# Kernel optimization log

Measured on AMD Instinct MI355X. Metric: run time of the kernel, lower is better.

Reference implementation:

```python
import jax, jax.numpy as jnp
import numpy as np

M_MARGIN = 0.5
S_SCALE = 30.0
EPS = 1e-12

def _l2norm(a):
    return a / jnp.maximum(jnp.linalg.norm(a, axis=1, keepdims=True), EPS)

def setup_inputs() -> dict:
    key = jax.random.key(0)
    k1, k2, k3 = jax.random.split(key, 3)
    B, D, V = 2048, 512, 32000
    x = jax.random.normal(k1, (B, D), dtype=jnp.float32)
    # kaiming_normal_ on (V, D): std = sqrt(2 / D)
    W = jax.random.normal(k2, (V, D), dtype=jnp.float32) * np.sqrt(2.0 / D)
    labels = jax.random.randint(k3, (B,), 0, V, dtype=jnp.int64)
    return {"x": x, "W": W, "labels": labels}

def reference(x, W, labels):
    cos_m, sin_m = jnp.cos(M_MARGIN), jnp.sin(M_MARGIN)
    nx = _l2norm(x)            # [B, D]
    nW = _l2norm(W)            # [V, D]
    cosine = nx @ nW.T         # [B, V]
    B = cosine.shape[0]
    rows = jnp.arange(B)
    # phi only matters at the label column (phi.where(one_hot, cosine))
    cos_y = cosine[rows, labels]                            # [B]
    sin_y = jnp.sqrt(jnp.clip(1.0 - cos_y * cos_y, 0.0, 1.0))
    phi_y = cos_y * cos_m - sin_y * sin_m                   # [B]
    logits = cosine.at[rows, labels].set(phi_y) * S_SCALE   # [B, V]
    logp = jax.nn.log_softmax(logits, axis=1)
    return -logp[rows, labels].sum() / B
```

## Files before the change

### kernel.cpp

```cpp
#include <hip/hip_runtime.h>
#include <math.h>
#include <stdint.h>

#define B_ROWS 2048
#define D_DIM  512
#define V_COLS 32000
#define BM 128
#define BN 128
#define BK 64
#define KSTEPS (D_DIM / BK)
#define NCT    (V_COLS / BN)
#define S_SC   30.0f
#define COS_M  0.8775825618903728f
#define SIN_M  0.479425538604203f

typedef float f32x4 __attribute__((ext_vector_type(4)));
typedef long  i64x2 __attribute__((ext_vector_type(2)));

__device__ __forceinline__ void load16_to_lds(const void* g, void* l) {
  __builtin_amdgcn_global_load_lds(
      (__attribute__((address_space(1))) void*)(g),
      (__attribute__((address_space(3))) void*)(l),
      16, 0, 0);
}

__global__ void fused_norm_kernel(const float* __restrict__ x,
                                  const float* __restrict__ W,
                                  uint8_t* __restrict__ nx,
                                  uint8_t* __restrict__ nw,
                                  float* __restrict__ rowsum,
                                  float* __restrict__ out) {
  if (blockIdx.x == 0 && threadIdx.x == 0) out[0] = 0.f;
  if (blockIdx.x < B_ROWS / 256) rowsum[blockIdx.x * 256 + threadIdx.x] = 0.f;
  const int lane = threadIdx.x & 63;
  const int wave = threadIdx.x >> 6;
  const int gr   = blockIdx.x * 4 + wave;
  const float* src;
  uint8_t* dst;
  if (gr < B_ROWS) {
    src = x + (size_t)gr * D_DIM;
    dst = nx + (size_t)gr * D_DIM;
  } else {
    src = W + (size_t)(gr - B_ROWS) * D_DIM;
    dst = nw + (size_t)(gr - B_ROWS) * D_DIM;
  }
  const float4* r4 = (const float4*)src;
  float4 v0 = r4[2 * lane];
  float4 v1 = r4[2 * lane + 1];
  float ss = v0.x*v0.x + v0.y*v0.y + v0.z*v0.z + v0.w*v0.w
           + v1.x*v1.x + v1.y*v1.y + v1.z*v1.z + v1.w*v1.w;
  #pragma unroll
  for (int off = 32; off >= 1; off >>= 1) ss += __shfl_xor(ss, off, 64);
  float inv = 1.0f / fmaxf(sqrtf(ss), 1e-12f);
  int p0 = __builtin_amdgcn_cvt_pk_fp8_f32(v0.x * inv, v0.y * inv, 0, false);
  p0     = __builtin_amdgcn_cvt_pk_fp8_f32(v0.z * inv, v0.w * inv, p0, true);
  int p1 = __builtin_amdgcn_cvt_pk_fp8_f32(v1.x * inv, v1.y * inv, 0, false);
  p1     = __builtin_amdgcn_cvt_pk_fp8_f32(v1.z * inv, v1.w * inv, p1, true);
  ((int2*)dst)[lane] = make_int2(p0, p1);
}

__global__ __launch_bounds__(256, 4)
void arc_gemm_kernel(const uint8_t* __restrict__ nx,
                     const uint8_t* __restrict__ nw,
                     const int* __restrict__ labels,
                     float* __restrict__ rowsum,
                     float* __restrict__ lbl_logit) {
  __shared__ uint8_t sA[2][BM * BK];
  __shared__ uint8_t sB[2][BN * BK];

  const int id = blockIdx.x;
  const int ct = ((id >> 7) << 3) | (id & 7);
  if (ct >= NCT) return;
  const int rt = (id >> 3) & 15;
  const int m0 = rt * BM;
  const int n0 = ct * BN;

  const int tid  = threadIdx.x;
  const int wave = tid >> 6;
  const int lane = tid & 63;
  const int wm   = wave >> 1;
  const int wn   = wave & 1;
  const int quad = lane >> 4;
  const int l16  = lane & 15;

  const int srow = tid >> 2;
  const int jg   = (tid & 3) ^ ((srow >> 1) & 3);
  const uint8_t* gA = nx + (size_t)(m0 + srow) * D_DIM + jg * 16;
  const uint8_t* gB = nw + (size_t)(n0 + srow) * D_DIM + jg * 16;
  const int ldsOff0 = wave * 1024;
  const int ldsOff1 = 4096 + wave * 1024;

  const int cSlot = (quad ^ ((l16 >> 1) & 3)) << 4;
  const int aBase = (wm * 64 + l16) * BK + cSlot;
  const int bBase = (wn * 64 + l16) * BK + cSlot;

  f32x4 acc[4][4];
  #pragma unroll
  for (int i = 0; i < 4; ++i)
    #pragma unroll
    for (int j = 0; j < 4; ++j) acc[i][j] = (f32x4){0.f, 0.f, 0.f, 0.f};

  load16_to_lds(gA,              &sA[0][ldsOff0]);
  load16_to_lds(gA + 64 * D_DIM, &sA[0][ldsOff1]);
  load16_to_lds(gB,              &sB[0][ldsOff0]);
  load16_to_lds(gB + 64 * D_DIM, &sB[0][ldsOff1]);

  #pragma unroll
  for (int ks = 0; ks < KSTEPS; ++ks) {
    __syncthreads();
    if (ks + 1 < KSTEPS) {
      const int off = (ks + 1) * BK;
      const int nb  = (ks + 1) & 1;
      load16_to_lds(gA + off,              &sA[nb][ldsOff0]);
      load16_to_lds(gA + 64 * D_DIM + off, &sA[nb][ldsOff1]);
      load16_to_lds(gB + off,              &sB[nb][ldsOff0]);
      load16_to_lds(gB + 64 * D_DIM + off, &sB[nb][ldsOff1]);
    }
    __syncthreads();

    const uint8_t* bA = sA[ks & 1];
    const uint8_t* bB = sB[ks & 1];
    i64x2 a2[4];
    #pragma unroll
    for (int mi = 0; mi < 4; ++mi)
      a2[mi] = *(const i64x2*)(bA + aBase + mi * 16 * BK);
    #pragma unroll
    for (int ni = 0; ni < 4; ++ni) {
      const i64x2 b2 = *(const i64x2*)(bB + bBase + ni * 16 * BK);
      #pragma unroll
      for (int mi = 0; mi < 4; ++mi) {
        acc[mi][ni] = __builtin_amdgcn_mfma_f32_16x16x32_fp8_fp8(a2[mi][0], b2[0], acc[mi][ni], 0, 0, 0);
        acc[mi][ni] = __builtin_amdgcn_mfma_f32_16x16x32_fp8_fp8(a2[mi][1], b2[1], acc[mi][ni], 0, 0, 0);
      }
    }
  }

  const int lblv = labels[m0 + wm * 64 + lane];
  #pragma unroll
  for (int mi = 0; mi < 4; ++mi) {
    #pragma unroll
    for (int r = 0; r < 4; ++r) {
      const int rw   = mi * 16 + quad * 4 + r;
      const int grow = m0 + wm * 64 + rw;
      const int lbl  = __shfl(lblv, rw, 64);
      float rsum = 0.f;
      #pragma unroll
      for (int ni = 0; ni < 4; ++ni) {
        float c = acc[mi][ni][r];
        const int gcol = n0 + wn * 64 + ni * 16 + l16;
        if (gcol == lbl) {
          float sy  = sqrtf(fminf(1.f, fmaxf(0.f, 1.f - c * c)));
          float phi = c * COS_M - sy * SIN_M;
          lbl_logit[grow] = S_SC * phi;
          c = phi;
        }
        rsum += __expf(S_SC * c - 30.0f);
      }
      #pragma unroll
      for (int off = 1; off < 16; off <<= 1)
        rsum += __shfl_xor(rsum, off, 64);
      if (l16 == 0) atomicAdd(&rowsum[grow], rsum);
    }
  }
}

__global__ void arc_finish_kernel(const float* __restrict__ rowsum,
                                  const float* __restrict__ lbl_logit,
                                  float* __restrict__ out) {
  const int row  = blockIdx.x * 256 + threadIdx.x;
  const int lane = threadIdx.x & 63;
  const int wave = threadIdx.x >> 6;
  float v = (30.0f + logf(rowsum[row]) - lbl_logit[row]) * (1.0f / (float)B_ROWS);
  #pragma unroll
  for (int off = 32; off >= 1; off >>= 1) v += __shfl_xor(v, off, 64);
  __shared__ float wsum[4];
  if (lane == 0) wsum[wave] = v;
  __syncthreads();
  if (threadIdx.x == 0) atomicAdd(out, wsum[0] + wsum[1] + wsum[2] + wsum[3]);
}

extern "C" void kernel_launch(void* const* d_in, const int* in_sizes, int n_in,
                              void* d_out, int out_size, void* d_ws, size_t ws_size,
                              hipStream_t stream) {
  const float* x      = (const float*)d_in[0];
  const float* W      = (const float*)d_in[1];
  const int*   labels = (const int*)d_in[2];
  float* out = (float*)d_out;

  char* ws = (char*)d_ws;
  uint8_t* nx = (uint8_t*)ws;
  uint8_t* nw = (uint8_t*)(ws + (size_t)B_ROWS * D_DIM);
  char* p = ws + (size_t)B_ROWS * D_DIM + (size_t)V_COLS * D_DIM;
  float* rowsum    = (float*)p;  p += (size_t)B_ROWS * 4;
  float* lbl_logit = (float*)p;

  hipLaunchKernelGGL(fused_norm_kernel, dim3((B_ROWS + V_COLS) / 4), dim3(256), 0, stream,
                     x, W, nx, nw, rowsum, out);
  hipLaunchKernelGGL(arc_gemm_kernel, dim3(32 * 16 * 8), dim3(256), 0, stream,
                     nx, nw, labels, rowsum, lbl_logit);
  hipLaunchKernelGGL(arc_finish_kernel, dim3(B_ROWS / 256), dim3(256), 0, stream,
                     rowsum, lbl_logit, out);
}
```

Baseline: 175.2 us.

## Switch GEMM to 32x32x64 scaled FP8 MFMA with 32-wide fragments

Replaces the 16x16x32 fp8 MFMA inner loop (32 instructions per k-step per wave) with four 32x32x64 mfma_scale f8f6f4 instructions, loading 32-byte A/B fragments from the swizzled LDS. The epilogue is remapped to the 32x32 accumulator layout, with a wider shuffle reduction and fewer atomics per row. Launch bounds drop to 3 blocks/SM to fit the larger register footprint. The aim is higher MFMA throughput and fewer LDS reads, at the cost of occupancy and a riskier fragment layout.

After: 295.2 us. 1.68x slower.

```diff
diff --git a/kernel.cpp b/kernel.cpp
--- a/kernel.cpp
+++ b/kernel.cpp
@@ -14,8 +14,9 @@
 #define COS_M  0.8775825618903728f
 #define SIN_M  0.479425538604203f
 
-typedef float f32x4 __attribute__((ext_vector_type(4)));
-typedef long  i64x2 __attribute__((ext_vector_type(2)));
+typedef float f32x16 __attribute__((ext_vector_type(16)));
+typedef int   i32x4v __attribute__((ext_vector_type(4)));
+typedef int   i32x8v __attribute__((ext_vector_type(8)));
 
 __device__ __forceinline__ void load16_to_lds(const void* g, void* l) {
   __builtin_amdgcn_global_load_lds(
@@ -59,7 +60,7 @@
   ((int2*)dst)[lane] = make_int2(p0, p1);
 }
 
-__global__ __launch_bounds__(256, 4)
+__global__ __launch_bounds__(256, 3)
 void arc_gemm_kernel(const uint8_t* __restrict__ nx,
                      const uint8_t* __restrict__ nw,
                      const int* __restrict__ labels,
@@ -80,8 +81,8 @@
   const int lane = tid & 63;
   const int wm   = wave >> 1;
   const int wn   = wave & 1;
-  const int quad = lane >> 4;
-  const int l16  = lane & 15;
+  const int c31  = lane & 31;
+  const int h    = lane >> 5;
 
   const int srow = tid >> 2;
   const int jg   = (tid & 3) ^ ((srow >> 1) & 3);
@@ -90,15 +91,18 @@
   const int ldsOff0 = wave * 1024;
   const int ldsOff1 = 4096 + wave * 1024;
 
-  const int cSlot = (quad ^ ((l16 >> 1) & 3)) << 4;
-  const int aBase = (wm * 64 + l16) * BK + cSlot;
-  const int bBase = (wn * 64 + l16) * BK + cSlot;
-
-  f32x4 acc[4][4];
-  #pragma unroll
-  for (int i = 0; i < 4; ++i)
+  const int swz  = (c31 >> 1) & 3;
+  const int s0   = ((2 * h) ^ swz) << 4;
+  const int aA0  = (wm * 64 + c31) * BK + s0;
+  const int bB0  = (wn * 64 + c31) * BK + s0;
+
+  f32x16 acc[2][2];
+  #pragma unroll
+  for (int i = 0; i < 2; ++i)
     #pragma unroll
-    for (int j = 0; j < 4; ++j) acc[i][j] = (f32x4){0.f, 0.f, 0.f, 0.f};
+    for (int j = 0; j < 2; ++j)
+      #pragma unroll
+      for (int g = 0; g < 16; ++g) acc[i][j][g] = 0.f;
 
   load16_to_lds(gA,              &sA[0][ldsOff0]);
   load16_to_lds(gA + 64 * D_DIM, &sA[0][ldsOff1]);
@@ -120,34 +124,39 @@
 
     const uint8_t* bA = sA[ks & 1];
     const uint8_t* bB = sB[ks & 1];
-    i64x2 a2[4];
+
+    i32x4v a0l = *(const i32x4v*)(bA + aA0);
+    i32x4v a0h = *(const i32x4v*)(bA + (aA0 ^ 16));
+    i32x4v a1l = *(const i32x4v*)(bA + aA0 + 32 * BK);
+    i32x4v a1h = *(const i32x4v*)(bA + ((aA0 + 32 * BK) ^ 16));
+    i32x4v b0l = *(const i32x4v*)(bB + bB0);
+    i32x4v b0h = *(const i32x4v*)(bB + (bB0 ^ 16));
+    i32x4v b1l = *(const i32x4v*)(bB + bB0 + 32 * BK);
+    i32x4v b1h = *(const i32x4v*)(bB + ((bB0 + 32 * BK) ^ 16));
+    i32x8v aF0 = __builtin_shufflevector(a0l, a0h, 0, 1, 2, 3, 4, 5, 6, 7);
+    i32x8v aF1 = __builtin_shufflevector(a1l, a1h, 0, 1, 2, 3, 4, 5, 6, 7);
+    i32x8v bF0 = __builtin_shufflevector(b0l, b0h, 0, 1, 2, 3, 4, 5, 6, 7);
+    i32x8v bF1 = __builtin_shufflevector(b1l, b1h, 0, 1, 2, 3, 4, 5, 6, 7);
+
+    acc[0][0] = __builtin_amdgcn_mfma_scale_f32_32x32x64_f8f6f4(aF0, bF0, acc[0][0], 0, 0, 0, 127, 0, 127);
+    acc[0][1] = __builtin_amdgcn_mfma_scale_f32_32x32x64_f8f6f4(aF0, bF1, acc[0][1], 0, 0, 0, 127, 0, 127);
+    acc[1][0] = __builtin_amdgcn_mfma_scale_f32_32x32x64_f8f6f4(aF1, bF0, acc[1][0], 0, 0, 0, 127, 0, 127);
+    acc[1][1] = __builtin_amdgcn_mfma_scale_f32_32x32x64_f8f6f4(aF1, bF1, acc[1][1], 0, 0, 0, 127, 0, 127);
+  }
+
+  const int lblv = labels[m0 + wm * 64 + lane];
+  #pragma unroll
+  for (int bi = 0; bi < 2; ++bi) {
     #pragma unroll
-    for (int mi = 0; mi < 4; ++mi)
-      a2[mi] = *(const i64x2*)(bA + aBase + mi * 16 * BK);
-    #pragma unroll
-    for (int ni = 0; ni < 4; ++ni) {
-      const i64x2 b2 = *(const i64x2*)(bB + bBase + ni * 16 * BK);
-      #pragma unroll
-      for (int mi = 0; mi < 4; ++mi) {
-        acc[mi][ni] = __builtin_amdgcn_mfma_f32_16x16x32_fp8_fp8(a2[mi][0], b2[0], acc[mi][ni], 0, 0, 0);
-        acc[mi][ni] = __builtin_amdgcn_mfma_f32_16x16x32_fp8_fp8(a2[mi][1], b2[1], acc[mi][ni], 0, 0, 0);
-      }
-    }
-  }
-
-  const int lblv = labels[m0 + wm * 64 + lane];
-  #pragma unroll
-  for (int mi = 0; mi < 4; ++mi) {
-    #pragma unroll
-    for (int r = 0; r < 4; ++r) {
-      const int rw   = mi * 16 + quad * 4 + r;
-      const int grow = m0 + wm * 64 + rw;
-      const int lbl  = __shfl(lblv, rw, 64);
+    for (int g = 0; g < 16; ++g) {
+      const int rr   = (g & 3) + ((g >> 2) << 3) + (h << 2);
+      const int grow = m0 + wm * 64 + bi * 32 + rr;
+      const int lbl  = __shfl(lblv, bi * 32 + rr, 64);
       float rsum = 0.f;
       #pragma unroll
-      for (int ni = 0; ni < 4; ++ni) {
-        float c = acc[mi][ni][r];
-        const int gcol = n0 + wn * 64 + ni * 16 + l16;
+      for (int bj = 0; bj < 2; ++bj) {
+        float c = acc[bi][bj][g];
+        const int gcol = n0 + wn * 64 + bj * 32 + c31;
         if (gcol == lbl) {
           float sy  = sqrtf(fminf(1.f, fmaxf(0.f, 1.f - c * c)));
           float phi = c * COS_M - sy * SIN_M;
@@ -157,9 +166,9 @@
         rsum += __expf(S_SC * c - 30.0f);
       }
       #pragma unroll
-      for (int off = 1; off < 16; off <<= 1)
+      for (int off = 1; off < 32; off <<= 1)
         rsum += __shfl_xor(rsum, off, 64);
-      if (l16 == 0) atomicAdd(&rowsum[grow], rsum);
+      if (c31 == 0) atomicAdd(&rowsum[grow], rsum);
     }
   }
 }
```
